# Kernel optimization log

Hardware: AMD Instinct MI355X
Metric: run time of the kernel (lower is better)

Reference implementation:

```python
import jax, jax.numpy as jnp
import numpy as np

B, N, DIN, DOUT = 8, 2048, 512, 512

def setup_inputs() -> dict:
    key = jax.random.key(0)
    kx, ka, kw, kb, kattn = jax.random.split(key, 5)
    x = jax.random.normal(kx, (B, N, DIN), dtype=jnp.float32)
    adjacency_matrix = jax.random.randint(ka, (B, N, N), 0, 2, dtype=jnp.int32)
    # nn.Linear(in,out): weight [out,in], bias [out]
    lim_w = float(np.sqrt(1.0 / DIN))
    W = jax.random.uniform(kw, (DOUT, DIN), minval=-lim_w, maxval=lim_w, dtype=jnp.float32)
    b = jax.random.uniform(kb, (DOUT,), minval=-lim_w, maxval=lim_w, dtype=jnp.float32)
    # xavier_uniform for attn [out,out]
    lim_a = float(np.sqrt(6.0 / (DOUT + DOUT)))
    attn = jax.random.uniform(kattn, (DOUT, DOUT), minval=-lim_a, maxval=lim_a, dtype=jnp.float32)
    return {"x": x, "adjacency_matrix": adjacency_matrix, "W": W, "b": b, "attn": attn}

def reference(x, adjacency_matrix, W, b, attn):
    h = jnp.einsum('bni,oi->bno', x, W) + b                 # [B,N,DOUT]
    ha = jnp.einsum('bmi,ij->bmj', h, attn)                  # h @ attn
    scores = jnp.einsum('bmj,bnj->bmn', ha, h)               # bilinear pairwise scores
    scores = jnp.where(adjacency_matrix == 0, -jnp.inf, scores)
    attn_weights = jax.nn.softmax(scores, axis=-1)           # adjacency-masked softmax
    x_out = jnp.einsum('bmn,bnd->bmd', attn_weights, h)      # weighted aggregation
    return jax.nn.elu(x_out)
```

## Files before the change

### kernel.cpp

```cpp
#include <hip/hip_runtime.h>
#include <cstdint>
#include <cstddef>

typedef unsigned short u16;
using f16x8 = __attribute__((ext_vector_type(8))) _Float16;
using f32x4 = __attribute__((ext_vector_type(4))) float;
using u16x4 = __attribute__((ext_vector_type(4))) unsigned short;

__device__ __forceinline__ u16 f2h(float f) {
  union { _Float16 h; u16 u; } c;
  c.h = (_Float16)f;
  return c.u;
}

__device__ __forceinline__ void gl_lds16(const void* g, void* lds) {
  __builtin_amdgcn_global_load_lds(
      (const __attribute__((address_space(1))) void*)(uintptr_t)g,
      (__attribute__((address_space(3))) void*)(uint32_t)(uintptr_t)lds,
      16, 0, 0);
}


template <int MODE>
__global__ __launch_bounds__(256) void gemm_bt(
    const u16* __restrict__ A, const u16* __restrict__ Bt,
    u16* __restrict__ C, const float* __restrict__ bias,
    u16* __restrict__ hTp, int Ncols, int K)
{
  __shared__ __align__(16) u16 sA[128 * 32];
  __shared__ __align__(16) u16 sB[128 * 32];

  const int m0 = blockIdx.y * 128;
  const int n0 = blockIdx.x * 128;
  const int t    = threadIdx.x;
  const int lane = t & 63;
  const int wave = t >> 6;
  const int wm   = (wave >> 1) * 64;
  const int wn   = (wave & 1) * 64;
  const int lm   = lane & 15;
  const int quad = lane >> 4;
  const int sw   = (quad ^ ((lm >> 1) & 3)) * 8;

  f32x4 acc[4][4];
#pragma unroll
  for (int i = 0; i < 4; ++i)
#pragma unroll
    for (int j = 0; j < 4; ++j) acc[i][j] = f32x4{0.f, 0.f, 0.f, 0.f};

  const int r0 = t >> 2,         c0 = t & 3;
  const int r1 = (t + 256) >> 2;
  const int g0 = c0 ^ ((r0 >> 1) & 3);
  const int g1 = c0 ^ ((r1 >> 1) & 3);
  const int ldsb0 = (t & ~63) * 8;
  const int ldsb1 = ((t & ~63) + 256) * 8;

  const int nk = K >> 5;
  for (int kc = 0; kc < nk; ++kc) {
    const int kb = kc * 32;
    gl_lds16(A  + (size_t)(m0 + r0) * K + kb + g0 * 8, sA + ldsb0);
    gl_lds16(A  + (size_t)(m0 + r1) * K + kb + g1 * 8, sA + ldsb1);
    gl_lds16(Bt + (size_t)(n0 + r0) * K + kb + g0 * 8, sB + ldsb0);
    gl_lds16(Bt + (size_t)(n0 + r1) * K + kb + g1 * 8, sB + ldsb1);
    __syncthreads();

    f16x8 af[4], bf[4];
#pragma unroll
    for (int i = 0; i < 4; ++i) {
      af[i] = *(const f16x8*)(sA + (wm + i * 16 + lm) * 32 + sw);
      bf[i] = *(const f16x8*)(sB + (wn + i * 16 + lm) * 32 + sw);
    }
#pragma unroll
    for (int i = 0; i < 4; ++i)
#pragma unroll
      for (int j = 0; j < 4; ++j)
        acc[i][j] = __builtin_amdgcn_mfma_f32_16x16x32_f16(af[i], bf[j], acc[i][j], 0, 0, 0);
    __syncthreads();
  }

#pragma unroll
  for (int j = 0; j < 4; ++j) {
    const int col = n0 + wn + j * 16 + lm;
    const float bv = bias ? bias[col] : 0.f;
#pragma unroll
    for (int i = 0; i < 4; ++i) {
      const int row0 = m0 + wm + i * 16 + quad * 4;
      u16x4 tp;
#pragma unroll
      for (int r = 0; r < 4; ++r) {
        const u16 hv = f2h(acc[i][j][r] + bv);
        C[(size_t)(row0 + r) * Ncols + col] = hv;
        tp[r] = hv;
      }
      if (MODE == 3) {
        const int b = row0 >> 11, n = row0 & 2047;
        *(u16x4*)(hTp + ((size_t)b * 512 + col) * 2048 + n) = tp;
      }
    }
  }
}

__global__ __launch_bounds__(256, 2) void flash_gat(
    const u16* __restrict__ haP, const u16* __restrict__ hP,
    const u16* __restrict__ hTP, const u16* __restrict__ adjb,
    float* __restrict__ outP)
{
  __shared__ __align__(16) u16 sQ[4 * 32 * 32];
  __shared__ __align__(16) u16 sK[4 * 128 * 32];
  __shared__ __align__(16) u16 sP[32 * 136];
  __shared__ float rmA[2][32], rsA[2][32];
  __shared__ float m_sh[32], l_sh[32], al_sh[32];

  const int t     = threadIdx.x;
  const int batch = blockIdx.x & 7;
  const int q0    = (blockIdx.x >> 3) << 5;
  const int lane  = t & 63;
  const int wave  = t >> 6;
  const int lm    = lane & 15;
  const int quad  = lane >> 4;
  const int sw    = (quad ^ ((lm >> 1) & 3)) * 8;
  const int wqm   = (wave >> 1) * 16;
  const int wqn   = (wave & 1) * 64;
  const int wd    = wave * 128;

  const u16* Q  = haP + ((size_t)batch * 2048 + q0) * 512;
  const u16* K  = hP  + (size_t)batch * 2048 * 512;
  const u16* V  = hTP + (size_t)batch * 512 * 2048;
  const u16* Ar = adjb + ((size_t)batch * 2048 + q0) * 128;
  float* Co = outP + ((size_t)batch * 2048 + q0) * 512;

  if (t < 32) { m_sh[t] = -1e30f; l_sh[t] = 0.f; }

  f32x4 o[2][8];
#pragma unroll
  for (int i = 0; i < 2; ++i)
#pragma unroll
    for (int j = 0; j < 8; ++j) o[i][j] = f32x4{0.f, 0.f, 0.f, 0.f};

  for (int nt = 0; nt < 16; ++nt) {
    const int n0 = nt * 128;
    f32x4 sacc[4];
#pragma unroll
    for (int j = 0; j < 4; ++j) sacc[j] = f32x4{0.f, 0.f, 0.f, 0.f};

    for (int kc = 0; kc < 4; ++kc) {
#pragma unroll
      for (int c = 0; c < 8; ++c) {
        const int s = c * 256 + t;
        const int q = s & 3, r = (s >> 2) & 127, pk = s >> 9;
        const int g = q ^ ((r >> 1) & 3);
        gl_lds16(K + (size_t)(n0 + r) * 512 + kc * 128 + pk * 32 + g * 8,
                 sK + (size_t)(c * 256 + (t & ~63)) * 8);
      }
#pragma unroll
      for (int c = 0; c < 2; ++c) {
        const int s = c * 256 + t;
        const int q = s & 3, r = (s >> 2) & 31, p = s >> 7;
        const int g = q ^ ((r >> 1) & 3);
        gl_lds16(Q + (size_t)r * 512 + kc * 128 + p * 32 + g * 8,
                 sQ + (size_t)(c * 256 + (t & ~63)) * 8);
      }
      __syncthreads();

#pragma unroll
      for (int kk = 0; kk < 4; ++kk) {
        const f16x8 aq = *(const f16x8*)(sQ + kk * 1024 + (wqm + lm) * 32 + sw);
        f16x8 bk[4];
#pragma unroll
        for (int j = 0; j < 4; ++j)
          bk[j] = *(const f16x8*)(sK + kk * 4096 + (wqn + j * 16 + lm) * 32 + sw);
#pragma unroll
        for (int j = 0; j < 4; ++j)
          sacc[j] = __builtin_amdgcn_mfma_f32_16x16x32_f16(aq, bk[j], sacc[j], 0, 0, 0);
      }
      __syncthreads();
    }

#pragma unroll
    for (int r = 0; r < 4; ++r) {
      const int R = wqm + quad * 4 + r;
      const u16x4 aw = *(const u16x4*)(Ar + (size_t)R * 128 + nt * 8 + (wqn >> 4));
      float mx = -1e30f;
#pragma unroll
      for (int j = 0; j < 4; ++j) {
        float s = sacc[j][r];
        s = ((aw[j] >> lm) & 1u) ? s : -1e30f;
        sacc[j][r] = s;
        mx = fmaxf(mx, s);
      }
      mx = fmaxf(mx, __shfl_xor(mx, 1));
      mx = fmaxf(mx, __shfl_xor(mx, 2));
      mx = fmaxf(mx, __shfl_xor(mx, 4));
      mx = fmaxf(mx, __shfl_xor(mx, 8));
      if (lm == 0) rmA[wave & 1][R] = mx;
    }
    __syncthreads();

#pragma unroll
    for (int r = 0; r < 4; ++r) {
      const int R = wqm + quad * 4 + r;
      const float cm = fmaxf(rmA[0][R], rmA[1][R]);
      const float nm = fmaxf(m_sh[R], cm);
      float rs = 0.f;
#pragma unroll
      for (int j = 0; j < 4; ++j) {
        const float p = __expf(sacc[j][r] - nm);
        rs += p;
        sP[R * 136 + wqn + j * 16 + lm] = f2h(p);
      }
      rs += __shfl_xor(rs, 1);
      rs += __shfl_xor(rs, 2);
      rs += __shfl_xor(rs, 4);
      rs += __shfl_xor(rs, 8);
      if (lm == 0) rsA[wave & 1][R] = rs;
    }
    __syncthreads();

    if (t < 32) {
      const float cm = fmaxf(rmA[0][t], rmA[1][t]);
      const float mo = m_sh[t];
      const float nm = fmaxf(mo, cm);
      const float a  = __expf(mo - nm);
      l_sh[t]  = a * l_sh[t] + rsA[0][t] + rsA[1][t];
      m_sh[t]  = nm;
      al_sh[t] = a;
    }
    __syncthreads();

#pragma unroll
    for (int i = 0; i < 2; ++i)
#pragma unroll
      for (int r = 0; r < 4; ++r) {
        const float a = al_sh[i * 16 + quad * 4 + r];
#pragma unroll
        for (int j = 0; j < 8; ++j) o[i][j][r] *= a;
      }
#pragma unroll
    for (int kb = 0; kb < 4; ++kb) {
      f16x8 ap[2], bv[8];
#pragma unroll
      for (int i = 0; i < 2; ++i)
        ap[i] = *(const f16x8*)(sP + (i * 16 + lm) * 136 + kb * 32 + quad * 8);
#pragma unroll
      for (int j = 0; j < 8; ++j)
        bv[j] = *(const f16x8*)(V + (size_t)(wd + j * 16 + lm) * 2048 + n0 + kb * 32 + quad * 8);
#pragma unroll
      for (int i = 0; i < 2; ++i)
#pragma unroll
        for (int j = 0; j < 8; ++j)
          o[i][j] = __builtin_amdgcn_mfma_f32_16x16x32_f16(ap[i], bv[j], o[i][j], 0, 0, 0);
    }
  }

#pragma unroll
  for (int i = 0; i < 2; ++i)
#pragma unroll
    for (int r = 0; r < 4; ++r) {
      const int R = i * 16 + quad * 4 + r;
      const float inv = 1.f / l_sh[R];
#pragma unroll
      for (int j = 0; j < 8; ++j) {
        float v = o[i][j][r] * inv;
        v = v > 0.f ? v : expm1f(v);
        Co[(size_t)R * 512 + wd + j * 16 + lm] = v;
      }
    }
}

__global__ __launch_bounds__(256) void adj_pack(
    const int* __restrict__ adj, u16* __restrict__ outw, int nwords)
{
  const int i = blockIdx.x * 256 + threadIdx.x;
  if (i >= nwords) return;
  const int4* p = (const int4*)(adj + (size_t)i * 16);
  unsigned w = 0;
#pragma unroll
  for (int k = 0; k < 4; ++k) {
    int4 v = p[k];
    w |= (unsigned)(v.x != 0) << (k * 4 + 0);
    w |= (unsigned)(v.y != 0) << (k * 4 + 1);
    w |= (unsigned)(v.z != 0) << (k * 4 + 2);
    w |= (unsigned)(v.w != 0) << (k * 4 + 3);
  }
  outw[i] = (u16)w;
}

__global__ __launch_bounds__(256) void cvt_f32_f16(
    const float* __restrict__ in, u16* __restrict__ outp, int n4)
{
  const int i = blockIdx.x * 256 + threadIdx.x;
  if (i >= n4) return;
  float4 v = ((const float4*)in)[i];
  u16x4 o; o[0] = f2h(v.x); o[1] = f2h(v.y); o[2] = f2h(v.z); o[3] = f2h(v.w);
  ((u16x4*)outp)[i] = o;
}

__global__ __launch_bounds__(256) void transpose_cvt(
    const float* __restrict__ in, u16* __restrict__ outp, int R, int C)
{
  const int idx = blockIdx.x * 256 + threadIdx.x;
  const int i = idx / C, j = idx % C;
  outp[(size_t)j * R + i] = f2h(in[idx]);
}

extern "C" void kernel_launch(void* const* d_in, const int* in_sizes, int n_in,
                              void* d_out, int out_size, void* d_ws, size_t ws_size,
                              hipStream_t stream) {
  (void)in_sizes; (void)n_in; (void)out_size;
  const float* x    = (const float*)d_in[0];
  const int*   adj  = (const int*)d_in[1];
  const float* W    = (const float*)d_in[2];
  const float* bvec = (const float*)d_in[3];
  const float* attn = (const float*)d_in[4];
  float* out = (float*)d_out;

  constexpr int B = 8, N = 2048, D = 512;
  constexpr size_t MN = (size_t)B * N;

  char* ws = (char*)d_ws;
  size_t off = 0;
  auto take = [&](size_t bytes) -> char* {
    char* p = ws + off;
    off += (bytes + 255) & ~(size_t)255;
    return p;
  };
  u16* xh   = (u16*)take(MN * D * 2);
  u16* Wh   = (u16*)take((size_t)D * D * 2);
  u16* attT = (u16*)take((size_t)D * D * 2);
  u16* h    = (u16*)take(MN * D * 2);
  u16* hT   = (u16*)take(MN * D * 2);
  u16* ha   = (u16*)take(MN * D * 2);
  u16* adjb = (u16*)take((size_t)B * N * (N / 16) * 2);
  if (off > ws_size) return;

  cvt_f32_f16<<<dim3((unsigned)(MN * D / 4 / 256)), 256, 0, stream>>>(x, xh, (int)(MN * D / 4));
  cvt_f32_f16<<<dim3(D * D / 4 / 256), 256, 0, stream>>>(W, Wh, D * D / 4);
  transpose_cvt<<<dim3(D * D / 256), 256, 0, stream>>>(attn, attT, D, D);
  const int nwords = (int)(MN * (N / 16));
  adj_pack<<<dim3(nwords / 256), 256, 0, stream>>>(adj, adjb, nwords);

  gemm_bt<3><<<dim3(D / 128, MN / 128), 256, 0, stream>>>(
      xh, Wh, h, bvec, hT, D, D);
  gemm_bt<0><<<dim3(D / 128, MN / 128), 256, 0, stream>>>(
      h, attT, ha, nullptr, nullptr, D, D);

  flash_gat<<<dim3(512), 256, 0, stream>>>(ha, h, hT, adjb, out);
}
```

Baseline: 488.8 us.

## Double-buffer K/Q staging in flash GAT and move to 8 waves per block

The flash attention kernel now runs 512 threads (8 waves) per block, each wave handling a smaller slice of scores and output columns. K and Q chunks are staged into a combined double-buffered LDS region so the next chunk's global-to-LDS load overlaps the current MFMAs, and the first chunk of the next tile is prefetched during the PV stage. The online-softmax running max and sum now live in per-thread registers instead of shared memory, which removes one barrier per tile. The cost is a 512-thread launch with a 4-blocks occupancy hint, which caps registers per thread, plus more complex staging index logic.

```diff
diff --git a/kernel.cpp b/kernel.cpp
--- a/kernel.cpp
+++ b/kernel.cpp
@@ -99,16 +99,15 @@
   }
 }
 
-__global__ __launch_bounds__(256, 2) void flash_gat(
+__global__ __launch_bounds__(512, 4) void flash_gat(
     const u16* __restrict__ haP, const u16* __restrict__ hP,
     const u16* __restrict__ hTP, const u16* __restrict__ adjb,
     float* __restrict__ outP)
 {
-  __shared__ __align__(16) u16 sQ[4 * 32 * 32];
-  __shared__ __align__(16) u16 sK[4 * 128 * 32];
+  __shared__ __align__(16) u16 sKQ[2 * 10240];
   __shared__ __align__(16) u16 sP[32 * 136];
-  __shared__ float rmA[2][32], rsA[2][32];
-  __shared__ float m_sh[32], l_sh[32], al_sh[32];
+  __shared__ __align__(16) float rmA2[32][4];
+  __shared__ __align__(16) float rsA2[32][4];
 
   const int t     = threadIdx.x;
   const int batch = blockIdx.x & 7;
@@ -118,135 +117,153 @@
   const int lm    = lane & 15;
   const int quad  = lane >> 4;
   const int sw    = (quad ^ ((lm >> 1) & 3)) * 8;
-  const int wqm   = (wave >> 1) * 16;
-  const int wqn   = (wave & 1) * 64;
-  const int wd    = wave * 128;
+  const int rg    = wave >> 2;
+  const int cg    = wave & 3;
+  const int wqm   = rg * 16;
+  const int wqn   = cg * 32;
+  const int wd    = wave * 64;
 
   const u16* Q  = haP + ((size_t)batch * 2048 + q0) * 512;
-  const u16* K  = hP  + (size_t)batch * 2048 * 512;
+  const u16* Kb = hP  + (size_t)batch * 2048 * 512;
   const u16* V  = hTP + (size_t)batch * 512 * 2048;
   const u16* Ar = adjb + ((size_t)batch * 2048 + q0) * 128;
   float* Co = outP + ((size_t)batch * 2048 + q0) * 512;
 
-  if (t < 32) { m_sh[t] = -1e30f; l_sh[t] = 0.f; }
-
-  f32x4 o[2][8];
+  const u16* sbase[3]; size_t sntm[3]; u16* sdst[3]; bool sact[3];
+#pragma unroll
+  for (int c = 0; c < 3; ++c) {
+    const int s = c * 512 + t;
+    sact[c] = (s < 1280);
+    const int q = s & 3, rr = s >> 2;
+    const int p = (rr >= 160) ? 1 : 0;
+    const int r = rr - p * 160;
+    const int g = q ^ ((r >> 1) & 3);
+    const bool isQ = (r >= 128);
+    sbase[c] = isQ ? (Q + (size_t)(r - 128) * 512 + p * 32 + g * 8)
+                   : (Kb + (size_t)r * 512 + p * 32 + g * 8);
+    sntm[c] = isQ ? 0 : (size_t)128 * 512;
+    sdst[c] = sKQ + (size_t)(c * 512 + (t & ~63)) * 8;
+  }
+
+  auto stage = [&](int ntv, int kc, int d) {
+    const size_t ko = (size_t)ntv * 0 + kc * 64;
+#pragma unroll
+    for (int c = 0; c < 3; ++c)
+      if (sact[c])
+        gl_lds16(sbase[c] + sntm[c] * ntv + ko, sdst[c] + d * 10240);
+  };
+
+  float m_[2][4], l_[2][4], al_[2][4];
 #pragma unroll
   for (int i = 0; i < 2; ++i)
 #pragma unroll
-    for (int j = 0; j < 8; ++j) o[i][j] = f32x4{0.f, 0.f, 0.f, 0.f};
+    for (int r = 0; r < 4; ++r) { m_[i][r] = -1e30f; l_[i][r] = 0.f; }
+
+  f32x4 o[2][4];
+#pragma unroll
+  for (int i = 0; i < 2; ++i)
+#pragma unroll
+    for (int j = 0; j < 4; ++j) o[i][j] = f32x4{0.f, 0.f, 0.f, 0.f};
+
+  stage(0, 0, 0);
 
   for (int nt = 0; nt < 16; ++nt) {
     const int n0 = nt * 128;
-    f32x4 sacc[4];
-#pragma unroll
-    for (int j = 0; j < 4; ++j) sacc[j] = f32x4{0.f, 0.f, 0.f, 0.f};
-
-    for (int kc = 0; kc < 4; ++kc) {
-#pragma unroll
-      for (int c = 0; c < 8; ++c) {
-        const int s = c * 256 + t;
-        const int q = s & 3, r = (s >> 2) & 127, pk = s >> 9;
-        const int g = q ^ ((r >> 1) & 3);
-        gl_lds16(K + (size_t)(n0 + r) * 512 + kc * 128 + pk * 32 + g * 8,
-                 sK + (size_t)(c * 256 + (t & ~63)) * 8);
-      }
-#pragma unroll
-      for (int c = 0; c < 2; ++c) {
-        const int s = c * 256 + t;
-        const int q = s & 3, r = (s >> 2) & 31, p = s >> 7;
-        const int g = q ^ ((r >> 1) & 3);
-        gl_lds16(Q + (size_t)r * 512 + kc * 128 + p * 32 + g * 8,
-                 sQ + (size_t)(c * 256 + (t & ~63)) * 8);
-      }
+    f32x4 sacc[2];
+    sacc[0] = f32x4{0.f, 0.f, 0.f, 0.f};
+    sacc[1] = f32x4{0.f, 0.f, 0.f, 0.f};
+
+    for (int kc = 0; kc < 8; ++kc) {
       __syncthreads();
-
-#pragma unroll
-      for (int kk = 0; kk < 4; ++kk) {
-        const f16x8 aq = *(const f16x8*)(sQ + kk * 1024 + (wqm + lm) * 32 + sw);
-        f16x8 bk[4];
-#pragma unroll
-        for (int j = 0; j < 4; ++j)
-          bk[j] = *(const f16x8*)(sK + kk * 4096 + (wqn + j * 16 + lm) * 32 + sw);
-#pragma unroll
-        for (int j = 0; j < 4; ++j)
-          sacc[j] = __builtin_amdgcn_mfma_f32_16x16x32_f16(aq, bk[j], sacc[j], 0, 0, 0);
-      }
-      __syncthreads();
-    }
-
+      if (kc < 7) stage(nt, kc + 1, (kc + 1) & 1);
+      const int b0 = (kc & 1) * 10240;
+#pragma unroll
+      for (int kk = 0; kk < 2; ++kk) {
+        const int pb = b0 + kk * 5120;
+        const f16x8 aq = *(const f16x8*)(sKQ + pb + (128 + wqm + lm) * 32 + sw);
+        const f16x8 bk0 = *(const f16x8*)(sKQ + pb + (wqn + lm) * 32 + sw);
+        const f16x8 bk1 = *(const f16x8*)(sKQ + pb + (wqn + 16 + lm) * 32 + sw);
+        sacc[0] = __builtin_amdgcn_mfma_f32_16x16x32_f16(aq, bk0, sacc[0], 0, 0, 0);
+        sacc[1] = __builtin_amdgcn_mfma_f32_16x16x32_f16(aq, bk1, sacc[1], 0, 0, 0);
+      }
+    }
+
+    const int awoff = nt * 8 + (wqn >> 4);
 #pragma unroll
     for (int r = 0; r < 4; ++r) {
       const int R = wqm + quad * 4 + r;
-      const u16x4 aw = *(const u16x4*)(Ar + (size_t)R * 128 + nt * 8 + (wqn >> 4));
-      float mx = -1e30f;
-#pragma unroll
-      for (int j = 0; j < 4; ++j) {
-        float s = sacc[j][r];
-        s = ((aw[j] >> lm) & 1u) ? s : -1e30f;
-        sacc[j][r] = s;
-        mx = fmaxf(mx, s);
-      }
+      const unsigned w = *(const unsigned*)(Ar + (size_t)R * 128 + awoff);
+      float s0 = ((w >> lm) & 1u) ? sacc[0][r] : -1e30f;
+      float s1 = ((w >> (lm + 16)) & 1u) ? sacc[1][r] : -1e30f;
+      sacc[0][r] = s0; sacc[1][r] = s1;
+      float mx = fmaxf(s0, s1);
       mx = fmaxf(mx, __shfl_xor(mx, 1));
       mx = fmaxf(mx, __shfl_xor(mx, 2));
       mx = fmaxf(mx, __shfl_xor(mx, 4));
       mx = fmaxf(mx, __shfl_xor(mx, 8));
-      if (lm == 0) rmA[wave & 1][R] = mx;
+      if (lm == 0) rmA2[R][cg] = mx;
     }
     __syncthreads();
 
 #pragma unroll
     for (int r = 0; r < 4; ++r) {
       const int R = wqm + quad * 4 + r;
-      const float cm = fmaxf(rmA[0][R], rmA[1][R]);
-      const float nm = fmaxf(m_sh[R], cm);
-      float rs = 0.f;
-#pragma unroll
-      for (int j = 0; j < 4; ++j) {
-        const float p = __expf(sacc[j][r] - nm);
-        rs += p;
-        sP[R * 136 + wqn + j * 16 + lm] = f2h(p);
-      }
+      const f32x4 rm = *(const f32x4*)rmA2[R];
+      const float cm = fmaxf(fmaxf(rm[0], rm[1]), fmaxf(rm[2], rm[3]));
+      const float mold = rg ? m_[1][r] : m_[0][r];
+      const float nm = fmaxf(mold, cm);
+      const float p0 = __expf(sacc[0][r] - nm);
+      const float p1 = __expf(sacc[1][r] - nm);
+      sP[R * 136 + wqn + lm]      = f2h(p0);
+      sP[R * 136 + wqn + 16 + lm] = f2h(p1);
+      float rs = p0 + p1;
       rs += __shfl_xor(rs, 1);
       rs += __shfl_xor(rs, 2);
       rs += __shfl_xor(rs, 4);
       rs += __shfl_xor(rs, 8);
-      if (lm == 0) rsA[wave & 1][R] = rs;
+      if (lm == 0) rsA2[R][cg] = rs;
     }
     __syncthreads();
 
-    if (t < 32) {
-      const float cm = fmaxf(rmA[0][t], rmA[1][t]);
-      const float mo = m_sh[t];
-      const float nm = fmaxf(mo, cm);
-      const float a  = __expf(mo - nm);
-      l_sh[t]  = a * l_sh[t] + rsA[0][t] + rsA[1][t];
-      m_sh[t]  = nm;
-      al_sh[t] = a;
-    }
-    __syncthreads();
-
 #pragma unroll
     for (int i = 0; i < 2; ++i)
 #pragma unroll
       for (int r = 0; r < 4; ++r) {
-        const float a = al_sh[i * 16 + quad * 4 + r];
-#pragma unroll
-        for (int j = 0; j < 8; ++j) o[i][j][r] *= a;
+        const int R = i * 16 + quad * 4 + r;
+        const f32x4 rm = *(const f32x4*)rmA2[R];
+        const f32x4 rs = *(const f32x4*)rsA2[R];
+        const float cm = fmaxf(fmaxf(rm[0], rm[1]), fmaxf(rm[2], rm[3]));
+        const float cs = (rs[0] + rs[1]) + (rs[2] + rs[3]);
+        const float nm = fmaxf(m_[i][r], cm);
+        const float a  = __expf(m_[i][r] - nm);
+        l_[i][r]  = a * l_[i][r] + cs;
+        m_[i][r]  = nm;
+        al_[i][r] = a;
+      }
+
+    stage((nt + 1) & 15, 0, 0);
+
+#pragma unroll
+    for (int i = 0; i < 2; ++i)
+#pragma unroll
+      for (int r = 0; r < 4; ++r) {
+        const float a = al_[i][r];
+#pragma unroll
+        for (int j = 0; j < 4; ++j) o[i][j][r] *= a;
       }
 #pragma unroll
     for (int kb = 0; kb < 4; ++kb) {
-      f16x8 ap[2], bv[8];
+      f16x8 ap[2], bv[4];
 #pragma unroll
       for (int i = 0; i < 2; ++i)
         ap[i] = *(const f16x8*)(sP + (i * 16 + lm) * 136 + kb * 32 + quad * 8);
 #pragma unroll
-      for (int j = 0; j < 8; ++j)
+      for (int j = 0; j < 4; ++j)
         bv[j] = *(const f16x8*)(V + (size_t)(wd + j * 16 + lm) * 2048 + n0 + kb * 32 + quad * 8);
 #pragma unroll
       for (int i = 0; i < 2; ++i)
 #pragma unroll
-        for (int j = 0; j < 8; ++j)
+        for (int j = 0; j < 4; ++j)
           o[i][j] = __builtin_amdgcn_mfma_f32_16x16x32_f16(ap[i], bv[j], o[i][j], 0, 0, 0);
     }
   }
@@ -256,9 +273,9 @@
 #pragma unroll
     for (int r = 0; r < 4; ++r) {
       const int R = i * 16 + quad * 4 + r;
-      const float inv = 1.f / l_sh[R];
-#pragma unroll
-      for (int j = 0; j < 8; ++j) {
+      const float inv = 1.f / l_[i][r];
+#pragma unroll
+      for (int j = 0; j < 4; ++j) {
         float v = o[i][j][r] * inv;
         v = v > 0.f ? v : expm1f(v);
         Co[(size_t)R * 512 + wd + j * 16 + lm] = v;
@@ -343,5 +360,5 @@
   gemm_bt<0><<<dim3(D / 128, MN / 128), 256, 0, stream>>>(
       h, attT, ha, nullptr, nullptr, D, D);
 
-  flash_gat<<<dim3(512), 256, 0, stream>>>(ha, h, hT, adjb, out);
-}
+  flash_gat<<<dim3(512), 512, 0, stream>>>(ha, h, hT, adjb, out);
+}
```

Result: slower. 710.2 us (+45.3%).
